# Optimization experiments

Measured on AMD Instinct MI355X. Metric: run time of the kernel, lower is better.

Reference implementation:

```python
import jax, jax.numpy as jnp
import numpy as np

B, S, H = 2, 2048, 2048
NH, NKV, HD = 16, 8, 128
EPS = 1e-6
THETA = 10000.0
SCALE = HD ** -0.5


def setup_inputs() -> dict:
    key = jax.random.key(0)
    ks = jax.random.split(key, 6)
    return {
        "positions": jnp.tile(jnp.arange(S, dtype=jnp.int64 if jax.config.jax_enable_x64 else jnp.int32), (B, 1)),
        "hidden_states": jax.random.normal(ks[0], (B, S, H), jnp.float32),
        "residual": jax.random.normal(ks[1], (B, S, H), jnp.float32),
        "layernorm_weight": 1.0 + 0.02 * jax.random.normal(ks[2], (H,), jnp.float32),
        "qkv_weight": 0.02 * jax.random.normal(ks[3], ((NH + 2 * NKV) * HD, H), jnp.float32),
        "o_weight": 0.02 * jax.random.normal(ks[4], (H, NH * HD), jnp.float32),
        "q_norm_weight": 1.0 + 0.02 * jax.random.normal(ks[5], (HD,), jnp.float32),
        "k_norm_weight": jnp.ones((HD,), jnp.float32),
    }


def _rmsnorm(x, w, eps=EPS):
    return x * jax.lax.rsqrt(jnp.mean(x * x, axis=-1, keepdims=True) + eps) * w


def _rope(x, positions):
    # x: [B, S, h, HD]; neox-style rotate-half RoPE
    inv_freq = 1.0 / (THETA ** (jnp.arange(0, HD, 2, dtype=jnp.float32) / HD))
    ang = positions.astype(jnp.float32)[..., None] * inv_freq  # [B, S, HD/2]
    cos = jnp.cos(ang)[:, :, None, :]
    sin = jnp.sin(ang)[:, :, None, :]
    x1, x2 = jnp.split(x, 2, axis=-1)
    return jnp.concatenate([x1 * cos - x2 * sin, x2 * cos + x1 * sin], axis=-1)


def reference(positions, hidden_states, residual, layernorm_weight,
              qkv_weight, o_weight, q_norm_weight, k_norm_weight):
    # Fused RMSNorm + QKV projection (on unnormalized hidden_states)
    xn = _rmsnorm(hidden_states, layernorm_weight)
    qkv = jnp.einsum('bsh,oh->bso', xn, qkv_weight)  # [B, S, (NH+2*NKV)*HD]
    q, k, v = jnp.split(qkv, [NH * HD, (NH + NKV) * HD], axis=-1)
    q = q.reshape(B, S, NH, HD)
    k = k.reshape(B, S, NKV, HD)
    v = v.reshape(B, S, NKV, HD)
    # per-head q/k RMSNorm (q_norm in fused QKV kernel, k_norm inside attention)
    q = _rmsnorm(q, q_norm_weight)
    k = _rmsnorm(k, k_norm_weight)
    # RoPE
    q = _rope(q, positions)
    k = _rope(k, positions)
    # GQA: expand KV heads
    rep = NH // NKV
    k = jnp.repeat(k, rep, axis=2)
    v = jnp.repeat(v, rep, axis=2)
    # causal attention
    scores = jnp.einsum('bqhd,bkhd->bhqk', q, k) * SCALE
    causal = jnp.tril(jnp.ones((S, S), bool))
    scores = jnp.where(causal[None, None], scores, jnp.finfo(scores.dtype).min)
    probs = jax.nn.softmax(scores, axis=-1)
    attn = jnp.einsum('bhqk,bkhd->bqhd', probs, v).reshape(B, S, NH * HD)
    # fused output projection + residual add
    return jnp.einsum('bsd,hd->bsh', attn, o_weight) + residual
```

## Files before the change

kernel.cpp:

```cpp
#include <hip/hip_runtime.h>
#include <hip/hip_bf16.h>

typedef __attribute__((ext_vector_type(8))) short bf16x8;
typedef __attribute__((ext_vector_type(4))) float f32x4;

#define B_ 2
#define S_ 2048
#define H_ 2048
#define NH_ 16
#define NKV_ 8
#define HD_ 128
#define M_ (B_ * S_)
#define NQKV_ ((NH_ + 2 * NKV_) * HD_)
#define QK_SCALE 0.08838834764831845f

#define VMCNT(n) asm volatile("s_waitcnt vmcnt(" #n ")" ::: "memory")

__device__ __forceinline__ unsigned short f2bf(float f) {
  unsigned int u = __float_as_uint(f);
  u += 0x7fffu + ((u >> 16) & 1u);
  return (unsigned short)(u >> 16);
}
__device__ __forceinline__ float bf2f(unsigned short h) {
  return __uint_as_float(((unsigned int)h) << 16);
}
__device__ __forceinline__ void gload_lds16(const void* g, void* l) {
  __builtin_amdgcn_global_load_lds(
      (const __attribute__((address_space(1))) void*)g,
      (__attribute__((address_space(3))) void*)l, 16, 0, 0);
}

__global__ __launch_bounds__(256) void k_rmsnorm(
    const float* __restrict__ x, const float* __restrict__ w,
    unsigned short* __restrict__ out) {
  __shared__ float red[4];
  const int m = blockIdx.x;
  const int t = threadIdx.x;
  const float4* row = (const float4*)(x + (size_t)m * H_);
  float4 v0 = row[t];
  float4 v1 = row[t + 256];
  float ss = v0.x * v0.x + v0.y * v0.y + v0.z * v0.z + v0.w * v0.w +
             v1.x * v1.x + v1.y * v1.y + v1.z * v1.z + v1.w * v1.w;
#pragma unroll
  for (int mk = 1; mk < 64; mk <<= 1) ss += __shfl_xor(ss, mk);
  if ((t & 63) == 0) red[t >> 6] = ss;
  __syncthreads();
  ss = red[0] + red[1] + red[2] + red[3];
  const float sc = rsqrtf(ss * (1.0f / H_) + 1e-6f);
  const float4* wv = (const float4*)w;
  float4 w0 = wv[t], w1 = wv[t + 256];
  ushort4 o0, o1;
  o0.x = f2bf(v0.x * sc * w0.x);
  o0.y = f2bf(v0.y * sc * w0.y);
  o0.z = f2bf(v0.z * sc * w0.z);
  o0.w = f2bf(v0.w * sc * w0.w);
  o1.x = f2bf(v1.x * sc * w1.x);
  o1.y = f2bf(v1.y * sc * w1.y);
  o1.z = f2bf(v1.z * sc * w1.z);
  o1.w = f2bf(v1.w * sc * w1.w);
  ushort4* orow = (ushort4*)(out + (size_t)m * H_);
  orow[t] = o0;
  orow[t + 256] = o1;
}

__global__ __launch_bounds__(256) void k_f32_to_bf16(
    const float* __restrict__ in, unsigned short* __restrict__ out, int n4) {
  int idx = blockIdx.x * 256 + threadIdx.x;
  const int stride = gridDim.x * 256;
  for (; idx < n4; idx += stride) {
    float4 v = ((const float4*)in)[idx];
    ushort4 o;
    o.x = f2bf(v.x);
    o.y = f2bf(v.y);
    o.z = f2bf(v.z);
    o.w = f2bf(v.w);
    ((ushort4*)out)[idx] = o;
  }
}

__global__ __launch_bounds__(256) void k_rope_table(
    const int* __restrict__ positions, float* __restrict__ cos_t,
    float* __restrict__ sin_t) {
  int idx = blockIdx.x * 256 + threadIdx.x;
  if (idx >= B_ * S_ * 64) return;
  int d = idx & 63;
  int bs = idx >> 6;
  float pos = (float)positions[bs];
  float inv_freq = powf(10000.0f, -(float)(2 * d) * (1.0f / HD_));
  float ang = pos * inv_freq;
  cos_t[idx] = cosf(ang);
  sin_t[idx] = sinf(ang);
}

template <int FMB, int FNB>
__device__ __forceinline__ void phase_loads(const unsigned short* sAb,
                                            const unsigned short* sBb, int wm,
                                            int wn, int lr, int lg,
                                            bf16x8 (&af)[2][4],
                                            bf16x8 (&bfv)[2][2]) {
#pragma unroll
  for (int kk = 0; kk < 2; ++kk) {
    const int pc = kk * 4 + lg;
#pragma unroll
    for (int i = 0; i < 4; ++i) {
      const int row = wm + (FMB + i) * 16 + lr;
      af[kk][i] = *(const bf16x8*)&sAb[row * 64 + ((pc ^ (row & 7)) << 3)];
    }
#pragma unroll
    for (int j = 0; j < 2; ++j) {
      const int row = wn + (FNB + j) * 16 + lr;
      bfv[kk][j] = *(const bf16x8*)&sBb[row * 64 + ((pc ^ (row & 7)) << 3)];
    }
  }
}

template <int FMB, int FNB>
__device__ __forceinline__ void phase_mfma(const bf16x8 (&af)[2][4],
                                           const bf16x8 (&bfv)[2][2],
                                           f32x4 (&acc)[8][4]) {
#pragma unroll
  for (int kk = 0; kk < 2; ++kk)
#pragma unroll
    for (int i = 0; i < 4; ++i)
#pragma unroll
      for (int j = 0; j < 2; ++j)
        acc[FMB + i][FNB + j] = __builtin_amdgcn_mfma_f32_16x16x32_bf16(
            af[kk][i], bfv[kk][j], acc[FMB + i][FNB + j], 0, 0, 0);
}

__global__ __launch_bounds__(512, 2) void k_gemm256(
    const unsigned short* __restrict__ A, const unsigned short* __restrict__ Bt,
    unsigned short* __restrict__ C, int M, int N, int K) {
  __shared__ unsigned short sA[2][256 * 64];
  __shared__ unsigned short sB[2][256 * 64];
  const int tid = threadIdx.x;
  const int w = tid >> 6;
  const int l = tid & 63;
  const int lr = l & 15, lg = l >> 4;
  const int gx = gridDim.x;
  const int lin = blockIdx.y * gx + blockIdx.x;
  const int cpx = (gx * gridDim.y) >> 3;
  const int swz = (lin & 7) * cpx + (lin >> 3);
  const int m0 = (swz / gx) * 256, n0 = (swz % gx) * 256;
  const int wm = (w >> 2) * 128, wn = (w & 3) * 64;
  f32x4 acc[8][4] = {};

  auto stageH = [&](int t, int bufi, int h) {
    const int k0 = t * 64;
    const unsigned short* src = (h < 2) ? A : Bt;
    unsigned short* dst = (h < 2) ? sA[bufi] : sB[bufi];
    const int rbase = (h & 1) * 128;
    const size_t gbase = (h < 2) ? (size_t)m0 : (size_t)n0;
#pragma unroll
    for (int i = 0; i < 2; ++i) {
      const int L = i * 512 + tid;
      const int r = L >> 3;
      const int p = L & 7;
      const int d = p ^ (r & 7);
      gload_lds16(src + (gbase + rbase + r) * (size_t)K + k0 + d * 8,
                  (char*)dst + (size_t)rbase * 128 +
                      (size_t)(i * 512 + w * 64) * 16);
    }
  };

#define GPHASE(FMB, FNB, DOSTAGE)                                       \
  {                                                                     \
    bf16x8 af[2][4];                                                    \
    bf16x8 bfv[2][2];                                                   \
    phase_loads<FMB, FNB>(sA[bufi], sB[bufi], wm, wn, lr, lg, af, bfv); \
    if (DOSTAGE && st) {                                                \
      stageH(t + 1, bufi ^ 1, 0);                                       \
      stageH(t + 1, bufi ^ 1, 1);                                       \
      stageH(t + 1, bufi ^ 1, 2);                                       \
      stageH(t + 1, bufi ^ 1, 3);                                       \
    }                                                                   \
    __builtin_amdgcn_s_barrier();                                       \
    asm volatile("s_waitcnt lgkmcnt(0)" ::: "memory");                  \
    __builtin_amdgcn_sched_barrier(0);                                  \
    __builtin_amdgcn_s_setprio(1);                                      \
    phase_mfma<FMB, FNB>(af, bfv, acc);                                 \
    __builtin_amdgcn_s_setprio(0);                                      \
  }

  stageH(0, 0, 0);
  stageH(0, 0, 1);
  stageH(0, 0, 2);
  stageH(0, 0, 3);
  VMCNT(0);
  __builtin_amdgcn_s_barrier();
  __builtin_amdgcn_sched_barrier(0);

  const int NT = K >> 6;
  for (int t = 0; t < NT; ++t) {
    const int bufi = t & 1;
    const bool st = (t + 1 < NT);
    GPHASE(0, 0, 1);
    __builtin_amdgcn_s_barrier();
    __builtin_amdgcn_sched_barrier(0);
    GPHASE(4, 0, 0);
    __builtin_amdgcn_s_barrier();
    __builtin_amdgcn_sched_barrier(0);
    GPHASE(4, 2, 0);
    __builtin_amdgcn_s_barrier();
    __builtin_amdgcn_sched_barrier(0);
    GPHASE(0, 2, 0);
    VMCNT(0);
    __builtin_amdgcn_s_barrier();
    __builtin_amdgcn_sched_barrier(0);
  }
#undef GPHASE

#pragma unroll
  for (int fm = 0; fm < 8; ++fm)
#pragma unroll
    for (int fn = 0; fn < 4; ++fn)
#pragma unroll
      for (int r = 0; r < 4; ++r) {
        const int row = m0 + wm + fm * 16 + lg * 4 + r;
        const int col = n0 + wn + fn * 16 + lr;
        C[(size_t)row * N + col] = f2bf(acc[fm][fn][r]);
      }
}

template <int FMB, int FNB>
__device__ __forceinline__ void phase_loads_o(const unsigned short* sAb,
                                              const unsigned short* sBb,
                                              int wm, int wn, int lr, int lg,
                                              bf16x8 (&af)[2][2],
                                              bf16x8 (&bfv)[2][2]) {
#pragma unroll
  for (int kk = 0; kk < 2; ++kk) {
    const int pc = kk * 4 + lg;
#pragma unroll
    for (int i = 0; i < 2; ++i) {
      const int row = wm + (FMB + i) * 16 + lr;
      af[kk][i] = *(const bf16x8*)&sAb[row * 64 + ((pc ^ (row & 7)) << 3)];
    }
#pragma unroll
    for (int j = 0; j < 2; ++j) {
      const int row = wn + (FNB + j) * 16 + lr;
      bfv[kk][j] = *(const bf16x8*)&sBb[row * 64 + ((pc ^ (row & 7)) << 3)];
    }
  }
}

template <int FMB, int FNB>
__device__ __forceinline__ void phase_mfma_o(const bf16x8 (&af)[2][2],
                                             const bf16x8 (&bfv)[2][2],
                                             f32x4 (&acc)[4][4]) {
#pragma unroll
  for (int kk = 0; kk < 2; ++kk)
#pragma unroll
    for (int i = 0; i < 2; ++i)
#pragma unroll
      for (int j = 0; j < 2; ++j)
        acc[FMB + i][FNB + j] = __builtin_amdgcn_mfma_f32_16x16x32_bf16(
            af[kk][i], bfv[kk][j], acc[FMB + i][FNB + j], 0, 0, 0);
}

__global__ __launch_bounds__(512, 1) void k_gemm_ores(
    const unsigned short* __restrict__ A, const unsigned short* __restrict__ Bt,
    float* __restrict__ Cout, const float* __restrict__ resid, int M, int N,
    int K) {
  __shared__ unsigned short sA[2][256 * 64];
  __shared__ unsigned short sB[2][128 * 64];
  const int tid = threadIdx.x;
  const int w = tid >> 6;
  const int l = tid & 63;
  const int lr = l & 15, lg = l >> 4;
  const int gx = gridDim.x;
  const int lin = blockIdx.y * gx + blockIdx.x;
  const int cpx = (gx * gridDim.y) >> 3;
  const int swz = (lin & 7) * cpx + (lin >> 3);
  const int m0 = (swz / gx) * 256, n0 = (swz % gx) * 128;
  const int wm = (w >> 1) * 64, wn = (w & 1) * 64;
  f32x4 acc[4][4] = {};

  auto stageH = [&](int t, int bufi, int h) {
    const int k0 = t * 64;
    const unsigned short* src = (h < 2) ? A : Bt;
    unsigned short* dst = (h < 2) ? sA[bufi] : sB[bufi];
    const int rbase = (h == 1) ? 128 : 0;
    const size_t gbase = (h < 2) ? (size_t)m0 : (size_t)n0;
#pragma unroll
    for (int i = 0; i < 2; ++i) {
      const int L = i * 512 + tid;
      const int r = L >> 3;
      const int p = L & 7;
      const int d = p ^ (r & 7);
      gload_lds16(src + (gbase + rbase + r) * (size_t)K + k0 + d * 8,
                  (char*)dst + (size_t)rbase * 128 +
                      (size_t)(i * 512 + w * 64) * 16);
    }
  };

#define OPHASE(FMB, FNB, DOSTAGE)                                         \
  {                                                                       \
    bf16x8 af[2][2];                                                      \
    bf16x8 bfv[2][2];                                                     \
    phase_loads_o<FMB, FNB>(sA[bufi], sB[bufi], wm, wn, lr, lg, af, bfv); \
    if (DOSTAGE && st) {                                                  \
      stageH(t + 1, bufi ^ 1, 0);                                         \
      stageH(t + 1, bufi ^ 1, 1);                                         \
      stageH(t + 1, bufi ^ 1, 2);                                         \
    }                                                                     \
    __builtin_amdgcn_s_barrier();                                         \
    asm volatile("s_waitcnt lgkmcnt(0)" ::: "memory");                    \
    __builtin_amdgcn_sched_barrier(0);                                    \
    __builtin_amdgcn_s_setprio(1);                                        \
    phase_mfma_o<FMB, FNB>(af, bfv, acc);                                 \
    __builtin_amdgcn_s_setprio(0);                                        \
  }

  stageH(0, 0, 0);
  stageH(0, 0, 1);
  stageH(0, 0, 2);
  VMCNT(0);
  __builtin_amdgcn_s_barrier();
  __builtin_amdgcn_sched_barrier(0);

  const int NT = K >> 6;
  for (int t = 0; t < NT; ++t) {
    const int bufi = t & 1;
    const bool st = (t + 1 < NT);
    OPHASE(0, 0, 1);
    __builtin_amdgcn_s_barrier();
    __builtin_amdgcn_sched_barrier(0);
    OPHASE(2, 0, 0);
    __builtin_amdgcn_s_barrier();
    __builtin_amdgcn_sched_barrier(0);
    OPHASE(2, 2, 0);
    __builtin_amdgcn_s_barrier();
    __builtin_amdgcn_sched_barrier(0);
    OPHASE(0, 2, 0);
    VMCNT(0);
    __builtin_amdgcn_s_barrier();
    __builtin_amdgcn_sched_barrier(0);
  }
#undef OPHASE

#pragma unroll
  for (int i = 0; i < 4; ++i)
#pragma unroll
    for (int j = 0; j < 4; ++j)
#pragma unroll
      for (int r = 0; r < 4; ++r) {
        const int row = m0 + wm + i * 16 + lg * 4 + r;
        const int col = n0 + wn + j * 16 + lr;
        const size_t o = (size_t)row * N + col;
        Cout[o] = acc[i][j][r] + resid[o];
      }
}

__global__ __launch_bounds__(256) void k_postprocess(
    const unsigned short* __restrict__ qkv, const float* __restrict__ qw,
    const float* __restrict__ kw, const float* __restrict__ cos_t,
    const float* __restrict__ sin_t, unsigned short* __restrict__ qb,
    unsigned short* __restrict__ kb, unsigned short* __restrict__ vb) {
  const int m = blockIdx.x;
  const int b = m >> 11, s = m & (S_ - 1);
  const int w = threadIdx.x >> 6, l = threadIdx.x & 63;
  const unsigned short* row = qkv + (size_t)m * NQKV_;
  const float c = cos_t[(size_t)m * 64 + l];
  const float sn = sin_t[(size_t)m * 64 + l];
  for (int hh = w * 8; hh < w * 8 + 8; ++hh) {
    int base, type;
    unsigned short* out;
    const float* nw;
    if (hh < NH_) {
      type = 0;
      base = hh * HD_;
      out = qb + ((size_t)(b * NH_ + hh) * S_ + s) * HD_;
      nw = qw;
    } else if (hh < NH_ + NKV_) {
      int kh = hh - NH_;
      type = 1;
      base = NH_ * HD_ + kh * HD_;
      out = kb + ((size_t)(b * NKV_ + kh) * S_ + s) * HD_;
      nw = kw;
    } else {
      int kh = hh - NH_ - NKV_;
      type = 2;
      base = (NH_ + NKV_) * HD_ + kh * HD_;
      out = vb + ((size_t)(b * NKV_ + kh) * S_ + s) * HD_;
      nw = nullptr;
    }
    unsigned short r1 = row[base + l];
    unsigned short r2 = row[base + 64 + l];
    if (type == 2) {
      out[l] = r1;
      out[64 + l] = r2;
      continue;
    }
    float x1 = bf2f(r1), x2 = bf2f(r2);
    float ss = x1 * x1 + x2 * x2;
#pragma unroll
    for (int mk = 1; mk < 64; mk <<= 1) ss += __shfl_xor(ss, mk);
    float sc = rsqrtf(ss * (1.0f / HD_) + 1e-6f);
    float y1 = x1 * sc * nw[l];
    float y2 = x2 * sc * nw[64 + l];
    float o1 = y1 * c - y2 * sn;
    float o2 = y2 * c + y1 * sn;
    if (type == 0) {
      o1 *= QK_SCALE;
      o2 *= QK_SCALE;
    }
    out[l] = f2bf(o1);
    out[64 + l] = f2bf(o2);
  }
}

__global__ __launch_bounds__(256) void k_transpose_v(
    const unsigned short* __restrict__ in,
    unsigned short* __restrict__ out) {
  __shared__ unsigned short tile[32][33];
  const int bx = blockIdx.x, by = blockIdx.y, bz = blockIdx.z;
  const unsigned short* src = in + (size_t)bz * S_ * HD_;
  unsigned short* dst = out + (size_t)bz * S_ * HD_;
  const int tx = threadIdx.x & 31, ty = threadIdx.x >> 5;
#pragma unroll
  for (int i = ty; i < 32; i += 8)
    tile[i][tx] = src[(size_t)(bx * 32 + i) * HD_ + by * 32 + tx];
  __syncthreads();
#pragma unroll
  for (int i = ty; i < 32; i += 8)
    dst[(size_t)(by * 32 + i) * S_ + bx * 32 + tx] = tile[tx][i];
}

#define MFIX 13.0f
__global__ __launch_bounds__(512, 4) void k_attn(
    const unsigned short* __restrict__ Q,
    const unsigned short* __restrict__ K,
    const unsigned short* __restrict__ VT,
    unsigned short* __restrict__ Oa) {
  __shared__ unsigned short kt[2][64 * 128];
  __shared__ unsigned short vt[2][128 * 64];
  __shared__ unsigned short pls[8 * 16 * 64];
  const int bh = blockIdx.y;
  const int b = bh >> 4, h = bh & 15;
  const int kvh = b * NKV_ + (h >> 1);
  const int xa = blockIdx.x;
  const int xb = 31 - xa;
  const int tid = threadIdx.x;
  const int w = tid >> 6, l = tid & 63;
  const int lr = l & 15, lg = l >> 4;
  const int wr = (w & 3) * 16;
  const int myx = (w < 4) ? xa : xb;
  const int q0m = myx * 64;

  bf16x8 qf[4];
  {
    const unsigned short* Qp = Q + ((size_t)bh * S_ + q0m + wr) * HD_;
#pragma unroll
    for (int tt = 0; tt < 4; ++tt)
      qf[tt] = *(const bf16x8*)(Qp + (size_t)lr * HD_ + tt * 32 + lg * 8);
  }
  f32x4 ao[8] = {};
  float lrow[4] = {0.f, 0.f, 0.f, 0.f};
  const unsigned short* Kp = K + (size_t)kvh * S_ * HD_;
  const unsigned short* Vp = VT + (size_t)kvh * HD_ * S_;
  unsigned short* pw = pls + w * 1024;

  auto stage = [&](int t, int bufi) {
    const int k0 = t * 64;
#pragma unroll
    for (int i = 0; i < 2; ++i) {
      const int chunk = i * 512 + tid;
      {
        const int r = chunk >> 4, p = chunk & 15;
        const int d = p ^ (r & 7);
        gload_lds16(Kp + (size_t)(k0 + r) * HD_ + d * 8,
                    (char*)kt[bufi] + (size_t)(i * 512 + w * 64) * 16);
      }
      {
        const int r = chunk >> 3, p = chunk & 7;
        const int d = p ^ (r & 7);
        gload_lds16(Vp + (size_t)r * S_ + k0 + d * 8,
                    (char*)vt[bufi] + (size_t)(i * 512 + w * 64) * 16);
      }
    }
  };

  auto process = [&](int t, int bufi, bool diag) {
    const unsigned short* ktb = kt[bufi];
    const unsigned short* vtb = vt[bufi];
    f32x4 sc[4] = {};
#pragma unroll
    for (int j = 0; j < 4; ++j)
#pragma unroll
      for (int tt = 0; tt < 4; ++tt) {
        bf16x8 kf = *(const bf16x8*)&ktb[(j * 16 + lr) * 128 +
                                         (((tt * 4 + lg) ^ (lr & 7)) << 3)];
        sc[j] =
            __builtin_amdgcn_mfma_f32_16x16x32_bf16(qf[tt], kf, sc[j], 0, 0, 0);
      }
    if (diag) {
      const int kvc = t * 64 + lr;
      const int qg = q0m + wr + lg * 4;
#pragma unroll
      for (int j = 0; j < 4; ++j)
#pragma unroll
        for (int r = 0; r < 4; ++r)
          if (kvc + j * 16 > qg + r) sc[j][r] = -1e30f;
    }
#pragma unroll
    for (int j = 0; j < 4; ++j)
#pragma unroll
      for (int r = 0; r < 4; ++r) {
        float p = __expf(sc[j][r] - MFIX);
        lrow[r] += p;
        const int row = lg * 4 + r;
        const int pchunk = ((j * 2) + (lr >> 3)) ^ (row & 7);
        pw[row * 64 + pchunk * 8 + (lr & 7)] = f2bf(p);
      }
#pragma unroll
    for (int ks = 0; ks < 2; ++ks) {
      bf16x8 pf =
          *(const bf16x8*)&pw[lr * 64 + (((ks * 4 + lg) ^ (lr & 7)) << 3)];
#pragma unroll
      for (int dj = 0; dj < 8; ++dj) {
        bf16x8 vf = *(const bf16x8*)&vtb[(dj * 16 + lr) * 64 +
                                         (((ks * 4 + lg) ^ (lr & 7)) << 3)];
        ao[dj] =
            __builtin_amdgcn_mfma_f32_16x16x32_bf16(pf, vf, ao[dj], 0, 0, 0);
      }
    }
  };

  stage(0, 0);
  __syncthreads();
  int cur = 0;
  for (int t = 0; t <= xb; ++t) {
    if (t < xb) stage(t + 1, cur ^ 1);
    if (t <= myx) process(t, cur, t == myx);
    __syncthreads();
    cur ^= 1;
  }

  float inv[4];
#pragma unroll
  for (int r = 0; r < 4; ++r) {
#pragma unroll
    for (int mk = 1; mk < 16; mk <<= 1) lrow[r] += __shfl_xor(lrow[r], mk);
    inv[r] = 1.0f / lrow[r];
  }
#pragma unroll
  for (int dj = 0; dj < 8; ++dj)
#pragma unroll
    for (int r = 0; r < 4; ++r) {
      const int sg = q0m + wr + lg * 4 + r;
      const size_t o =
          ((size_t)b * S_ + sg) * (NH_ * HD_) + h * HD_ + dj * 16 + lr;
      Oa[o] = f2bf(ao[dj][r] * inv[r]);
    }
}

extern "C" void kernel_launch(void* const* d_in, const int* in_sizes, int n_in,
                              void* d_out, int out_size, void* d_ws,
                              size_t ws_size, hipStream_t stream) {
  const int* positions = (const int*)d_in[0];
  const float* hidden = (const float*)d_in[1];
  const float* residual = (const float*)d_in[2];
  const float* ln_w = (const float*)d_in[3];
  const float* qkv_w = (const float*)d_in[4];
  const float* o_w = (const float*)d_in[5];
  const float* q_nw = (const float*)d_in[6];
  const float* k_nw = (const float*)d_in[7];

  char* ws = (char*)d_ws;
  const size_t SZ_XN = (size_t)M_ * H_ * 2;
  const size_t SZ_QKVW = (size_t)NQKV_ * H_ * 2;
  const size_t SZ_OW = (size_t)H_ * (NH_ * HD_) * 2;
  const size_t SZ_QKV = (size_t)M_ * NQKV_ * 2;
  const size_t SZ_KB = (size_t)B_ * NKV_ * S_ * HD_ * 2;
  const size_t SZ_COS = (size_t)B_ * S_ * 64 * 4;

  unsigned short* xn = (unsigned short*)(ws);
  unsigned short* q_buf = (unsigned short*)(ws);
  unsigned short* qkvw_bf = (unsigned short*)(ws + SZ_XN);
  unsigned short* k_buf = (unsigned short*)(ws + SZ_XN);
  unsigned short* v_buf = (unsigned short*)(ws + SZ_XN + SZ_KB);
  unsigned short* owbf = (unsigned short*)(ws + SZ_XN + SZ_QKVW);
  unsigned short* qkv_bf = (unsigned short*)(ws + SZ_XN + SZ_QKVW + SZ_OW);
  unsigned short* attn_o = qkv_bf;
  unsigned short* vt_buf =
      (unsigned short*)(ws + SZ_XN + SZ_QKVW + SZ_OW + SZ_QKV);
  float* cos_t = (float*)(ws + SZ_XN + SZ_QKVW + SZ_OW + SZ_QKV + SZ_KB);
  float* sin_t = (float*)((char*)cos_t + SZ_COS);

  k_rmsnorm<<<M_, 256, 0, stream>>>(hidden, ln_w, xn);
  k_f32_to_bf16<<<2048, 256, 0, stream>>>(qkv_w, qkvw_bf,
                                          (int)(SZ_QKVW / 2 / 4));
  k_f32_to_bf16<<<1024, 256, 0, stream>>>(o_w, owbf, (int)(SZ_OW / 2 / 4));
  k_rope_table<<<(B_ * S_ * 64) / 256, 256, 0, stream>>>(positions, cos_t,
                                                         sin_t);
  k_gemm256<<<dim3(NQKV_ / 256, M_ / 256), 512, 0, stream>>>(
      xn, qkvw_bf, qkv_bf, M_, NQKV_, H_);
  k_postprocess<<<M_, 256, 0, stream>>>(qkv_bf, q_nw, k_nw, cos_t, sin_t,
                                        q_buf, k_buf, v_buf);
  k_transpose_v<<<dim3(S_ / 32, HD_ / 32, B_ * NKV_), 256, 0, stream>>>(v_buf,
                                                                        vt_buf);
  k_attn<<<dim3(16, B_ * NH_), 512, 0, stream>>>(q_buf, k_buf, vt_buf, attn_o);
  k_gemm_ores<<<dim3((NH_ * HD_) / 128, M_ / 256), 512, 0, stream>>>(
      attn_o, owbf, (float*)d_out, residual, M_, NH_ * HD_, H_);
}
```

Measured before the change: 251.1 us.

## Spread next-tile global loads across GEMM phases with partial vmcnt waits

Both GEMM kernels now issue the global-to-LDS loads for the next K tile in four chunks, one per MFMA phase, instead of all at once in the first phase. The LDS layout is reordered so each chunk fills the rows that a given phase reads. Partial vmcnt waits replace the single full wait at the end of each iteration. The aim is to smooth memory traffic and overlap it more evenly with MFMA work, at the cost of more complex ordering that could race if the vmcnt counts are off.

```diff
diff --git a/kernel.cpp b/kernel.cpp
--- a/kernel.cpp
+++ b/kernel.cpp
@@ -103,13 +103,19 @@
     const int pc = kk * 4 + lg;
 #pragma unroll
     for (int i = 0; i < 4; ++i) {
-      const int row = wm + (FMB + i) * 16 + lr;
-      af[kk][i] = *(const bf16x8*)&sAb[row * 64 + ((pc ^ (row & 7)) << 3)];
+      const int R = wm + (FMB + i) * 16 + lr;
+      const int idx = ((R >> 6) & 1) * 8192 +
+                      ((((R >> 7) << 6) | (R & 63)) << 6) +
+                      ((pc ^ (R & 7)) << 3);
+      af[kk][i] = *(const bf16x8*)&sAb[idx];
     }
 #pragma unroll
     for (int j = 0; j < 2; ++j) {
-      const int row = wn + (FNB + j) * 16 + lr;
-      bfv[kk][j] = *(const bf16x8*)&sBb[row * 64 + ((pc ^ (row & 7)) << 3)];
+      const int R = wn + (FNB + j) * 16 + lr;
+      const int idx = ((R >> 5) & 1) * 8192 +
+                      ((((R >> 6) << 5) | (R & 31)) << 6) +
+                      ((pc ^ (R & 7)) << 3);
+      bfv[kk][j] = *(const bf16x8*)&sBb[idx];
     }
   }
 }
@@ -145,35 +151,39 @@
   const int wm = (w >> 2) * 128, wn = (w & 3) * 64;
   f32x4 acc[8][4] = {};
 
-  auto stageH = [&](int t, int bufi, int h) {
+  auto stageA = [&](int t, int bufi, int h) {
     const int k0 = t * 64;
-    const unsigned short* src = (h < 2) ? A : Bt;
-    unsigned short* dst = (h < 2) ? sA[bufi] : sB[bufi];
-    const int rbase = (h & 1) * 128;
-    const size_t gbase = (h < 2) ? (size_t)m0 : (size_t)n0;
 #pragma unroll
     for (int i = 0; i < 2; ++i) {
       const int L = i * 512 + tid;
       const int r = L >> 3;
-      const int p = L & 7;
-      const int d = p ^ (r & 7);
-      gload_lds16(src + (gbase + rbase + r) * (size_t)K + k0 + d * 8,
-                  (char*)dst + (size_t)rbase * 128 +
+      const int R = ((r >> 6) << 7) | (h << 6) | (r & 63);
+      const int d = (L & 7) ^ (r & 7);
+      gload_lds16(A + (size_t)(m0 + R) * K + k0 + d * 8,
+                  (char*)sA[bufi] + h * 16384 +
                       (size_t)(i * 512 + w * 64) * 16);
     }
   };
-
-#define GPHASE(FMB, FNB, DOSTAGE)                                       \
+  auto stageB = [&](int t, int bufi, int h) {
+    const int k0 = t * 64;
+#pragma unroll
+    for (int i = 0; i < 2; ++i) {
+      const int L = i * 512 + tid;
+      const int r = L >> 3;
+      const int R = ((r >> 5) << 6) | (h << 5) | (r & 31);
+      const int d = (L & 7) ^ (r & 7);
+      gload_lds16(Bt + (size_t)(n0 + R) * K + k0 + d * 8,
+                  (char*)sB[bufi] + h * 16384 +
+                      (size_t)(i * 512 + w * 64) * 16);
+    }
+  };
+
+#define GPHASE(FMB, FNB, STAGECALL)                                     \
   {                                                                     \
     bf16x8 af[2][4];                                                    \
     bf16x8 bfv[2][2];                                                   \
     phase_loads<FMB, FNB>(sA[bufi], sB[bufi], wm, wn, lr, lg, af, bfv); \
-    if (DOSTAGE && st) {                                                \
-      stageH(t + 1, bufi ^ 1, 0);                                       \
-      stageH(t + 1, bufi ^ 1, 1);                                       \
-      stageH(t + 1, bufi ^ 1, 2);                                       \
-      stageH(t + 1, bufi ^ 1, 3);                                       \
-    }                                                                   \
+    STAGECALL;                                                          \
     __builtin_amdgcn_s_barrier();                                       \
     asm volatile("s_waitcnt lgkmcnt(0)" ::: "memory");                  \
     __builtin_amdgcn_sched_barrier(0);                                  \
@@ -182,10 +192,10 @@
     __builtin_amdgcn_s_setprio(0);                                      \
   }
 
-  stageH(0, 0, 0);
-  stageH(0, 0, 1);
-  stageH(0, 0, 2);
-  stageH(0, 0, 3);
+  stageA(0, 0, 0);
+  stageB(0, 0, 0);
+  stageA(0, 0, 1);
+  stageB(0, 0, 1);
   VMCNT(0);
   __builtin_amdgcn_s_barrier();
   __builtin_amdgcn_sched_barrier(0);
@@ -193,18 +203,29 @@
   const int NT = K >> 6;
   for (int t = 0; t < NT; ++t) {
     const int bufi = t & 1;
+    const int nb = bufi ^ 1;
     const bool st = (t + 1 < NT);
-    GPHASE(0, 0, 1);
-    __builtin_amdgcn_s_barrier();
-    __builtin_amdgcn_sched_barrier(0);
-    GPHASE(4, 0, 0);
-    __builtin_amdgcn_s_barrier();
-    __builtin_amdgcn_sched_barrier(0);
-    GPHASE(4, 2, 0);
-    __builtin_amdgcn_s_barrier();
-    __builtin_amdgcn_sched_barrier(0);
-    GPHASE(0, 2, 0);
-    VMCNT(0);
+    GPHASE(0, 0, if (st) stageA(t + 1, nb, 0));
+    if (st) {
+      VMCNT(4);
+    } else {
+      VMCNT(2);
+    }
+    __builtin_amdgcn_s_barrier();
+    __builtin_amdgcn_sched_barrier(0);
+    GPHASE(4, 0, if (st) stageB(t + 1, nb, 0));
+    if (st) {
+      VMCNT(4);
+    } else {
+      VMCNT(0);
+    }
+    __builtin_amdgcn_s_barrier();
+    __builtin_amdgcn_sched_barrier(0);
+    GPHASE(4, 2, if (st) stageA(t + 1, nb, 1));
+    __builtin_amdgcn_s_barrier();
+    __builtin_amdgcn_sched_barrier(0);
+    GPHASE(0, 2, if (st) stageB(t + 1, nb, 1));
+    if (st) VMCNT(4);
     __builtin_amdgcn_s_barrier();
     __builtin_amdgcn_sched_barrier(0);
   }
@@ -233,13 +254,19 @@
     const int pc = kk * 4 + lg;
 #pragma unroll
     for (int i = 0; i < 2; ++i) {
-      const int row = wm + (FMB + i) * 16 + lr;
-      af[kk][i] = *(const bf16x8*)&sAb[row * 64 + ((pc ^ (row & 7)) << 3)];
+      const int R = wm + (FMB + i) * 16 + lr;
+      const int idx = ((R >> 5) & 1) * 8192 +
+                      ((((R >> 6) << 5) | (R & 31)) << 6) +
+                      ((pc ^ (R & 7)) << 3);
+      af[kk][i] = *(const bf16x8*)&sAb[idx];
     }
 #pragma unroll
     for (int j = 0; j < 2; ++j) {
-      const int row = wn + (FNB + j) * 16 + lr;
-      bfv[kk][j] = *(const bf16x8*)&sBb[row * 64 + ((pc ^ (row & 7)) << 3)];
+      const int R = wn + (FNB + j) * 16 + lr;
+      const int idx = ((R >> 5) & 1) * 4096 +
+                      ((((R >> 6) << 5) | (R & 31)) << 6) +
+                      ((pc ^ (R & 7)) << 3);
+      bfv[kk][j] = *(const bf16x8*)&sBb[idx];
     }
   }
 }
@@ -276,34 +303,35 @@
   const int wm = (w >> 1) * 64, wn = (w & 1) * 64;
   f32x4 acc[4][4] = {};
 
-  auto stageH = [&](int t, int bufi, int h) {
+  auto stageAo = [&](int t, int bufi, int h) {
     const int k0 = t * 64;
-    const unsigned short* src = (h < 2) ? A : Bt;
-    unsigned short* dst = (h < 2) ? sA[bufi] : sB[bufi];
-    const int rbase = (h == 1) ? 128 : 0;
-    const size_t gbase = (h < 2) ? (size_t)m0 : (size_t)n0;
 #pragma unroll
     for (int i = 0; i < 2; ++i) {
       const int L = i * 512 + tid;
       const int r = L >> 3;
-      const int p = L & 7;
-      const int d = p ^ (r & 7);
-      gload_lds16(src + (gbase + rbase + r) * (size_t)K + k0 + d * 8,
-                  (char*)dst + (size_t)rbase * 128 +
+      const int R = ((r >> 5) << 6) | (h << 5) | (r & 31);
+      const int d = (L & 7) ^ (r & 7);
+      gload_lds16(A + (size_t)(m0 + R) * K + k0 + d * 8,
+                  (char*)sA[bufi] + h * 16384 +
                       (size_t)(i * 512 + w * 64) * 16);
     }
   };
-
-#define OPHASE(FMB, FNB, DOSTAGE)                                         \
+  auto stageBo = [&](int t, int bufi, int h) {
+    const int k0 = t * 64;
+    const int L = tid;
+    const int r = L >> 3;
+    const int R = ((r >> 5) << 6) | (h << 5) | (r & 31);
+    const int d = (L & 7) ^ (r & 7);
+    gload_lds16(Bt + (size_t)(n0 + R) * K + k0 + d * 8,
+                (char*)sB[bufi] + h * 8192 + (size_t)(w * 64) * 16);
+  };
+
+#define OPHASE(FMB, FNB, STAGECALL)                                       \
   {                                                                       \
     bf16x8 af[2][2];                                                      \
     bf16x8 bfv[2][2];                                                     \
     phase_loads_o<FMB, FNB>(sA[bufi], sB[bufi], wm, wn, lr, lg, af, bfv); \
-    if (DOSTAGE && st) {                                                  \
-      stageH(t + 1, bufi ^ 1, 0);                                         \
-      stageH(t + 1, bufi ^ 1, 1);                                         \
-      stageH(t + 1, bufi ^ 1, 2);                                         \
-    }                                                                     \
+    STAGECALL;                                                            \
     __builtin_amdgcn_s_barrier();                                         \
     asm volatile("s_waitcnt lgkmcnt(0)" ::: "memory");                    \
     __builtin_amdgcn_sched_barrier(0);                                    \
@@ -312,9 +340,10 @@
     __builtin_amdgcn_s_setprio(0);                                        \
   }
 
-  stageH(0, 0, 0);
-  stageH(0, 0, 1);
-  stageH(0, 0, 2);
+  stageAo(0, 0, 0);
+  stageBo(0, 0, 0);
+  stageAo(0, 0, 1);
+  stageBo(0, 0, 1);
   VMCNT(0);
   __builtin_amdgcn_s_barrier();
   __builtin_amdgcn_sched_barrier(0);
@@ -322,18 +351,29 @@
   const int NT = K >> 6;
   for (int t = 0; t < NT; ++t) {
     const int bufi = t & 1;
+    const int nb = bufi ^ 1;
     const bool st = (t + 1 < NT);
-    OPHASE(0, 0, 1);
-    __builtin_amdgcn_s_barrier();
-    __builtin_amdgcn_sched_barrier(0);
-    OPHASE(2, 0, 0);
-    __builtin_amdgcn_s_barrier();
-    __builtin_amdgcn_sched_barrier(0);
-    OPHASE(2, 2, 0);
-    __builtin_amdgcn_s_barrier();
-    __builtin_amdgcn_sched_barrier(0);
-    OPHASE(0, 2, 0);
-    VMCNT(0);
+    OPHASE(0, 0, if (st) stageAo(t + 1, nb, 0));
+    if (st) {
+      VMCNT(3);
+    } else {
+      VMCNT(1);
+    }
+    __builtin_amdgcn_s_barrier();
+    __builtin_amdgcn_sched_barrier(0);
+    OPHASE(2, 0, if (st) stageBo(t + 1, nb, 0));
+    if (st) {
+      VMCNT(3);
+    } else {
+      VMCNT(0);
+    }
+    __builtin_amdgcn_s_barrier();
+    __builtin_amdgcn_sched_barrier(0);
+    OPHASE(2, 2, if (st) stageAo(t + 1, nb, 1));
+    __builtin_amdgcn_s_barrier();
+    __builtin_amdgcn_sched_barrier(0);
+    OPHASE(0, 2, if (st) stageBo(t + 1, nb, 1));
+    if (st) VMCNT(3);
     __builtin_amdgcn_s_barrier();
     __builtin_amdgcn_sched_barrier(0);
   }
```

New measurement: 248.8 us. Within noise of the previous version (-0.9%).
